# Performance work log

Hardware: AMD Instinct MI355X
Metric: run time of the kernel (lower is better)

Reference implementation:

```python
import jax, jax.numpy as jnp
import numpy as np

N = 16384
E = 524288
F_IN, F_HID, F_OUT = 128, 256, 128
EPS = 1e-5


def setup_inputs() -> dict:
    key = jax.random.key(0)
    ks = jax.random.split(key, 8)
    x = jax.random.normal(ks[0], (N, F_IN), dtype=jnp.float32)
    edge_index = jax.random.randint(ks[1], (2, E), 0, N, dtype=jnp.int64)
    edge_weight = jax.random.uniform(ks[2], (E,), dtype=jnp.float32)
    # Linear params stored as [in, out] (y = x @ W + b; same math as torch Linear)
    W1_w = jax.random.normal(ks[3], (F_IN, F_HID), dtype=jnp.float32) / np.sqrt(F_IN)
    W1_b = jnp.zeros((F_HID,), dtype=jnp.float32)
    W2_w = jax.random.normal(ks[4], (F_HID, F_OUT), dtype=jnp.float32) / np.sqrt(F_HID)
    W2_b = jnp.zeros((F_OUT,), dtype=jnp.float32)
    ln_g = jnp.ones((F_HID,), dtype=jnp.float32)
    ln_b = jnp.zeros((F_HID,), dtype=jnp.float32)
    return {"x": x, "edge_index": edge_index, "edge_weight": edge_weight,
            "W1_w": W1_w, "W1_b": W1_b, "W2_w": W2_w, "W2_b": W2_b,
            "ln_g": ln_g, "ln_b": ln_b}


def _layernorm(h, g, b):
    mu = jnp.mean(h, axis=-1, keepdims=True)
    var = jnp.var(h, axis=-1, keepdims=True)
    return (h - mu) * jax.lax.rsqrt(var + EPS) * g + b


def reference(x, edge_index, edge_weight, W1_w, W1_b, W2_w, W2_b, ln_g, ln_b):
    n = x.shape[0]
    adj = jnp.zeros((n, n), dtype=x.dtype).at[edge_index[0], edge_index[1]].set(edge_weight)
    adj = adj + jnp.eye(n, dtype=x.dtype)
    degree = jnp.clip(adj.sum(axis=1, keepdims=True), 1.0, None)
    adj = adj / degree
    h = jnp.matmul(adj, x) @ W1_w + W1_b          # [N, F_HID]
    h = jax.nn.relu(_layernorm(h, ln_g, ln_b))
    # dropout is identity in eval mode
    out = jnp.matmul(adj, h) @ W2_w + W2_b        # [N, F_OUT]
    return out
```

## Files before the change

kernel.cpp:

```cpp
#include <hip/hip_runtime.h>

#define N_NODES 16384
#define F_IN    128
#define F_HID   256
#define F_OUT   128
#define LN_EPS  1e-5f
#define CAP     96
#define H0STR   136
#define H1STR   264
#define REPSTR  132

typedef __attribute__((ext_vector_type(8))) short bf16x8;
typedef __attribute__((ext_vector_type(4))) float f32x4;
typedef __attribute__((ext_vector_type(4))) int   i32x4;
typedef __attribute__((ext_vector_type(4))) unsigned u32x4;

__device__ __forceinline__ unsigned short bf16rne(float f) {
    unsigned u = __float_as_uint(f);
    unsigned r = (u + 0x7fffu + ((u >> 16) & 1u)) >> 16;
    return (unsigned short)r;
}
__device__ __forceinline__ float bf_lo(unsigned v) { return __uint_as_float(v << 16); }
__device__ __forceinline__ float bf_hi(unsigned v) { return __uint_as_float(v & 0xffff0000u); }

__global__ void pre_small_kernel(int* __restrict__ cur, const unsigned* __restrict__ ei,
                                 int* __restrict__ mode) {
    int b = blockIdx.x, t = threadIdx.x;
    if (b < 64) {
        cur[b * 256 + t] = 0;
    } else {
        __shared__ int nz;
        if (t == 0) nz = 0;
        __syncthreads();
        for (int it = 0; it < 4; ++it) {
            int idx = 2 * (t + it * 256) + 1;
            if (ei[idx] != 0u) nz = 1;
        }
        __syncthreads();
        if (t == 0) *mode = (nz == 0) ? 1 : 0;
    }
}

__global__ void prep_fill_kernel(const void* __restrict__ ei, const int* __restrict__ mode,
                                 int* __restrict__ cur, int2* __restrict__ ed, int E, int nF,
                                 const float* __restrict__ x, unsigned short* __restrict__ xb,
                                 const float* __restrict__ W1, unsigned short* __restrict__ W1t,
                                 const float* __restrict__ W2, unsigned short* __restrict__ W2t) {
    int b = blockIdx.x, t = threadIdx.x;
    if (b < nF) {
        int base = b * 1024 + t;
        int m = *mode;
#pragma unroll
        for (int u = 0; u < 4; ++u) {
            int e = base + u * 256;
            if (e >= E) continue;
            int r, c;
            if (m) {
                const long long* p = (const long long*)ei;
                r = (int)p[e]; c = (int)p[e + E];
            } else {
                const int* p = (const int*)ei;
                r = p[e]; c = p[e + E];
            }
            if (((unsigned)r | (unsigned)c) >= N_NODES) continue;
            int pos = atomicAdd(&cur[r], 1);
            if (pos < CAP) ed[r * CAP + pos] = make_int2(c, e);
        }
    } else if (b < nF + 2048) {
        int i = ((b - nF) * 256 + t) * 4;
        float4 v = *(const float4*)&x[i];
        ushort4 o;
        o.x = bf16rne(v.x); o.y = bf16rne(v.y); o.z = bf16rne(v.z); o.w = bf16rne(v.w);
        *(ushort4*)&xb[i] = o;
    } else if (b < nF + 2176) {
        int id = (b - nF - 2048) * 256 + t;
        int n = id >> 7, k = id & 127;
        W1t[id] = bf16rne(W1[(size_t)k * F_HID + n]);
    } else {
        int id = (b - nF - 2176) * 256 + t;
        int n = id >> 8, k = id & 255;
        W2t[id] = bf16rne(W2[(size_t)k * F_OUT + n]);
    }
}

__launch_bounds__(1024, 8)
__global__ void agg_mlp_kernel(const float* __restrict__ ew, int* __restrict__ cur,
                               int2* __restrict__ ed, float* __restrict__ invdeg,
                               const unsigned* __restrict__ xb,
                               const unsigned short* __restrict__ W1t,
                               const unsigned short* __restrict__ W2t,
                               const float* __restrict__ b1,
                               const float* __restrict__ ln_g, const float* __restrict__ ln_b,
                               unsigned short* __restrict__ h2b) {
    __shared__ int   scol[16][CAP];
    __shared__ int   seid[16][CAP];
    __shared__ float sw[16][CAP];
    __shared__ unsigned short H0[16 * H0STR];
    __shared__ unsigned short H1[16 * H1STR];
    __shared__ float red[2][16][16];

    int t = threadIdx.x, wave = t >> 6, lane = t & 63;
    int lnid = lane & 15, quad = lane >> 4;
    int qw = lane >> 4, ql = lane & 15;
    int Rbase = blockIdx.x * 16;
    int r = Rbase + wave;

    int d = cur[r];
    if (d > CAP) d = CAP;
    int dpad = (d + 15) & ~15;
    int2* row = ed + (size_t)r * CAP;
    for (int i = lane; i < d; i += 64) {
        int2 e = row[i];
        scol[wave][i] = e.x;
        seid[wave][i] = e.y;
    }
    for (int i = d + lane; i < dpad; i += 64) {
        scol[wave][i] = -2;
        seid[wave][i] = 0;
    }
    asm volatile("s_waitcnt lgkmcnt(0)" ::: "memory");

    float wsum = 0.0f;
    for (int i = lane; i < d; i += 64) {
        int myc = scol[wave][i], mye = seid[wave][i];
        bool kill = false;
        for (int jb = 0; jb < dpad; jb += 16) {
            const int* cb = &scol[wave][jb];
            const int* eb = &seid[wave][jb];
            i32x4 c0 = *(const i32x4*)(cb);
            i32x4 c1 = *(const i32x4*)(cb + 4);
            i32x4 c2 = *(const i32x4*)(cb + 8);
            i32x4 c3 = *(const i32x4*)(cb + 12);
            i32x4 e0 = *(const i32x4*)(eb);
            i32x4 e1 = *(const i32x4*)(eb + 4);
            i32x4 e2 = *(const i32x4*)(eb + 8);
            i32x4 e3 = *(const i32x4*)(eb + 12);
            kill |= (c0.x == myc && e0.x > mye);
            kill |= (c0.y == myc && e0.y > mye);
            kill |= (c0.z == myc && e0.z > mye);
            kill |= (c0.w == myc && e0.w > mye);
            kill |= (c1.x == myc && e1.x > mye);
            kill |= (c1.y == myc && e1.y > mye);
            kill |= (c1.z == myc && e1.z > mye);
            kill |= (c1.w == myc && e1.w > mye);
            kill |= (c2.x == myc && e2.x > mye);
            kill |= (c2.y == myc && e2.y > mye);
            kill |= (c2.z == myc && e2.z > mye);
            kill |= (c2.w == myc && e2.w > mye);
            kill |= (c3.x == myc && e3.x > mye);
            kill |= (c3.y == myc && e3.y > mye);
            kill |= (c3.z == myc && e3.z > mye);
            kill |= (c3.w == myc && e3.w > mye);
        }
        float w = kill ? 0.0f : ew[mye];
        sw[wave][i] = w;
        row[i] = make_int2(myc, __float_as_int(w));
        wsum += w;
    }
    asm volatile("s_waitcnt lgkmcnt(0)" ::: "memory");
    for (int off = 32; off; off >>= 1) wsum += __shfl_xor(wsum, off, 64);
    float inv = 1.0f / (1.0f + wsum);
    if (lane == 0) { invdeg[r] = inv; cur[r] = d; }

    const u32x4* xb4 = (const u32x4*)xb;
    float a[8] = {0, 0, 0, 0, 0, 0, 0, 0};
    int j = 0;
    for (; j + 16 <= d; j += 16) {
        int c[4]; float w[4]; u32x4 v[4];
#pragma unroll
        for (int u = 0; u < 4; ++u) {
            int n = j + u * 4 + qw;
            c[u] = scol[wave][n];
            w[u] = sw[wave][n];
        }
#pragma unroll
        for (int u = 0; u < 4; ++u) v[u] = xb4[(size_t)c[u] * 16 + ql];
#pragma unroll
        for (int u = 0; u < 4; ++u)
#pragma unroll
            for (int m = 0; m < 4; ++m) {
                a[2 * m]     += w[u] * bf_lo(v[u][m]);
                a[2 * m + 1] += w[u] * bf_hi(v[u][m]);
            }
    }
    for (; j + 4 <= d; j += 4) {
        int n = j + qw;
        int c = scol[wave][n];
        float w = sw[wave][n];
        u32x4 v = xb4[(size_t)c * 16 + ql];
#pragma unroll
        for (int m = 0; m < 4; ++m) {
            a[2 * m]     += w * bf_lo(v[m]);
            a[2 * m + 1] += w * bf_hi(v[m]);
        }
    }
    int rem = d - j;
    if (rem > 0) {
        int n = j + (qw < rem ? qw : 0);
        float w = (qw < rem) ? sw[wave][n] : 0.0f;
        int c = scol[wave][n];
        u32x4 v = xb4[(size_t)c * 16 + ql];
#pragma unroll
        for (int m = 0; m < 4; ++m) {
            a[2 * m]     += w * bf_lo(v[m]);
            a[2 * m + 1] += w * bf_hi(v[m]);
        }
    }
#pragma unroll
    for (int k = 0; k < 8; ++k) {
        a[k] += __shfl_xor(a[k], 16, 64);
        a[k] += __shfl_xor(a[k], 32, 64);
    }
    if (qw == 0) {
        u32x4 sv = xb4[(size_t)r * 16 + ql];
        u32x4 o;
#pragma unroll
        for (int m = 0; m < 4; ++m) {
            float lo = (a[2 * m]     + bf_lo(sv[m])) * inv;
            float hi = (a[2 * m + 1] + bf_hi(sv[m])) * inv;
            o[m] = ((unsigned)bf16rne(hi) << 16) | (unsigned)bf16rne(lo);
        }
        *(u32x4*)&H0[wave * H0STR + ql * 8] = o;
    }
    __syncthreads();

    bf16x8 afr[4];
#pragma unroll
    for (int ch = 0; ch < 4; ++ch)
        afr[ch] = *(const bf16x8*)&H0[lnid * H0STR + ch * 32 + quad * 8];
    f32x4 acc = {0.0f, 0.0f, 0.0f, 0.0f};
    {
        const unsigned short* wrow = &W1t[(size_t)(wave * 16 + lnid) * F_IN];
#pragma unroll
        for (int ch = 0; ch < 4; ++ch) {
            bf16x8 b = *(const bf16x8*)&wrow[ch * 32 + quad * 8];
            acc = __builtin_amdgcn_mfma_f32_16x16x32_bf16(afr[ch], b, acc, 0, 0, 0);
        }
    }
    float s[4], q[4];
    {
        float bv = b1[wave * 16 + lnid];
#pragma unroll
        for (int rr = 0; rr < 4; ++rr) {
            float v = acc[rr] + bv;
            acc[rr] = v;
            s[rr] = v; q[rr] = v * v;
        }
    }
#pragma unroll
    for (int rr = 0; rr < 4; ++rr)
        for (int off = 1; off < 16; off <<= 1) {
            s[rr] += __shfl_xor(s[rr], off, 64);
            q[rr] += __shfl_xor(q[rr], off, 64);
        }
    if (lnid == 0) {
#pragma unroll
        for (int rr = 0; rr < 4; ++rr) {
            red[0][wave][quad * 4 + rr] = s[rr];
            red[1][wave][quad * 4 + rr] = q[rr];
        }
    }
    __syncthreads();
    float mean[4], rinv[4];
#pragma unroll
    for (int rr = 0; rr < 4; ++rr) {
        int rowi = quad * 4 + rr;
        float S = 0.0f, Q = 0.0f;
#pragma unroll
        for (int w2 = 0; w2 < 16; ++w2) { S += red[0][w2][rowi]; Q += red[1][w2][rowi]; }
        mean[rr] = S * (1.0f / F_HID);
        float var = Q * (1.0f / F_HID) - mean[rr] * mean[rr];
        rinv[rr] = rsqrtf(var + LN_EPS);
    }
    {
        int c = wave * 16 + lnid;
        float g = ln_g[c], bb = ln_b[c];
#pragma unroll
        for (int rr = 0; rr < 4; ++rr) {
            float v = fmaxf((acc[rr] - mean[rr]) * rinv[rr] * g + bb, 0.0f);
            H1[(quad * 4 + rr) * H1STR + c] = bf16rne(v);
        }
    }
    __syncthreads();

    unsigned short* rep = H0;
    if (wave < 8) {
        bf16x8 a2[8];
#pragma unroll
        for (int ch = 0; ch < 8; ++ch)
            a2[ch] = *(const bf16x8*)&H1[lnid * H1STR + ch * 32 + quad * 8];
        f32x4 c2 = {0.0f, 0.0f, 0.0f, 0.0f};
        const unsigned short* wrow = &W2t[(size_t)(wave * 16 + lnid) * F_HID];
#pragma unroll
        for (int ch = 0; ch < 8; ++ch) {
            bf16x8 b = *(const bf16x8*)&wrow[ch * 32 + quad * 8];
            c2 = __builtin_amdgcn_mfma_f32_16x16x32_bf16(a2[ch], b, c2, 0, 0, 0);
        }
#pragma unroll
        for (int rr = 0; rr < 4; ++rr)
            rep[(quad * 4 + rr) * REPSTR + wave * 16 + lnid] = bf16rne(c2[rr]);
    }
    __syncthreads();

    if (t < 512) {
        int m = t >> 5, cg = t & 31;
        *(ushort4*)&h2b[(size_t)(Rbase + m) * F_OUT + cg * 4] =
            *(const ushort4*)&rep[m * REPSTR + cg * 4];
    }
}

__launch_bounds__(1024, 8)
__global__ void spmm2_kernel(const unsigned* __restrict__ xb, const int* __restrict__ cur,
                             const int2* __restrict__ ed, const float* __restrict__ invdeg,
                             const float* __restrict__ bias, float* __restrict__ outp) {
    __shared__ int   scol[16][CAP];
    __shared__ float sw[16][CAP];
    int t = threadIdx.x, wave = t >> 6, lane = t & 63;
    int qw = lane >> 4, ql = lane & 15;
    int r = blockIdx.x * 16 + wave;
    const int2* row = ed + (size_t)r * CAP;
    int d = cur[r];
    if (d > CAP) d = CAP;
    for (int i = lane; i < d; i += 64) {
        int2 e = row[i];
        scol[wave][i] = e.x;
        sw[wave][i] = __int_as_float(e.y);
    }
    asm volatile("s_waitcnt lgkmcnt(0)" ::: "memory");

    const u32x4* xb4 = (const u32x4*)xb;
    float a[8] = {0, 0, 0, 0, 0, 0, 0, 0};
    int j = 0;
    for (; j + 16 <= d; j += 16) {
        int c[4]; float w[4]; u32x4 v[4];
#pragma unroll
        for (int u = 0; u < 4; ++u) {
            int n = j + u * 4 + qw;
            c[u] = scol[wave][n];
            w[u] = sw[wave][n];
        }
#pragma unroll
        for (int u = 0; u < 4; ++u) v[u] = xb4[(size_t)c[u] * 16 + ql];
#pragma unroll
        for (int u = 0; u < 4; ++u)
#pragma unroll
            for (int m = 0; m < 4; ++m) {
                a[2 * m]     += w[u] * bf_lo(v[u][m]);
                a[2 * m + 1] += w[u] * bf_hi(v[u][m]);
            }
    }
    for (; j + 4 <= d; j += 4) {
        int n = j + qw;
        int c = scol[wave][n];
        float w = sw[wave][n];
        u32x4 v = xb4[(size_t)c * 16 + ql];
#pragma unroll
        for (int m = 0; m < 4; ++m) {
            a[2 * m]     += w * bf_lo(v[m]);
            a[2 * m + 1] += w * bf_hi(v[m]);
        }
    }
    int rem = d - j;
    if (rem > 0) {
        int n = j + (qw < rem ? qw : 0);
        float w = (qw < rem) ? sw[wave][n] : 0.0f;
        int c = scol[wave][n];
        u32x4 v = xb4[(size_t)c * 16 + ql];
#pragma unroll
        for (int m = 0; m < 4; ++m) {
            a[2 * m]     += w * bf_lo(v[m]);
            a[2 * m + 1] += w * bf_hi(v[m]);
        }
    }
#pragma unroll
    for (int k = 0; k < 8; ++k) {
        a[k] += __shfl_xor(a[k], 16, 64);
        a[k] += __shfl_xor(a[k], 32, 64);
    }
    if (qw == 0) {
        float inv = invdeg[r];
        u32x4 sv = xb4[(size_t)r * 16 + ql];
        int f = ql * 8;
        f32x4 o0, o1;
#pragma unroll
        for (int m = 0; m < 2; ++m) {
            o0[2 * m]     = (a[2 * m]     + bf_lo(sv[m])) * inv + bias[f + 2 * m];
            o0[2 * m + 1] = (a[2 * m + 1] + bf_hi(sv[m])) * inv + bias[f + 2 * m + 1];
        }
#pragma unroll
        for (int m = 2; m < 4; ++m) {
            o1[2 * m - 4] = (a[2 * m]     + bf_lo(sv[m])) * inv + bias[f + 2 * m];
            o1[2 * m - 3] = (a[2 * m + 1] + bf_hi(sv[m])) * inv + bias[f + 2 * m + 1];
        }
        *(f32x4*)&outp[(size_t)r * F_OUT + f]     = o0;
        *(f32x4*)&outp[(size_t)r * F_OUT + f + 4] = o1;
    }
}

extern "C" void kernel_launch(void* const* d_in, const int* in_sizes, int n_in,
                              void* d_out, int out_size, void* d_ws, size_t ws_size,
                              hipStream_t stream) {
    const float* x   = (const float*)d_in[0];
    const void*  ei  = d_in[1];
    const float* ew  = (const float*)d_in[2];
    const float* W1  = (const float*)d_in[3];
    const float* b1  = (const float*)d_in[4];
    const float* W2  = (const float*)d_in[5];
    const float* b2  = (const float*)d_in[6];
    const float* lng = (const float*)d_in[7];
    const float* lnb = (const float*)d_in[8];
    float* out = (float*)d_out;
    int E = in_sizes[2];

    char* w = (char*)d_ws;
    size_t off = 0;
    auto take = [&](size_t bytes) -> char* {
        char* p = w + off;
        off += (bytes + 255) & ~(size_t)255;
        return p;
    };
    int*   cur    = (int*)take((size_t)N_NODES * 4);
    float* invdeg = (float*)take((size_t)N_NODES * 4);
    int2*  ed     = (int2*)take((size_t)N_NODES * CAP * 8);
    unsigned short* xb  = (unsigned short*)take((size_t)N_NODES * F_IN * 2);
    unsigned short* h2b = (unsigned short*)take((size_t)N_NODES * F_OUT * 2);
    unsigned short* W1t = (unsigned short*)take((size_t)F_IN * F_HID * 2);
    unsigned short* W2t = (unsigned short*)take((size_t)F_HID * F_OUT * 2);
    int*   mode   = (int*)take(4);

    int nF = (E + 1023) / 1024;
    pre_small_kernel<<<65, 256, 0, stream>>>(cur, (const unsigned*)ei, mode);
    prep_fill_kernel<<<nF + 2304, 256, 0, stream>>>(ei, mode, cur, ed, E, nF,
                                                    x, xb, W1, W1t, W2, W2t);
    agg_mlp_kernel<<<N_NODES / 16, 1024, 0, stream>>>(ew, cur, ed, invdeg,
                                                      (const unsigned*)xb, W1t, W2t,
                                                      b1, lng, lnb, h2b);
    spmm2_kernel<<<N_NODES / 16, 1024, 0, stream>>>((const unsigned*)h2b, cur, ed, invdeg,
                                                    b2, out);
}
```

Baseline: 185.3 us.

## Split feature dimension into two planes for cache-friendly sparse aggregation passes

Stores the bf16 node features and the second-layer hidden features as two 64-column planes, and runs each neighbor-gather aggregation as a separate kernel per plane. Each plane is 2 MB instead of 4 MB, so the random gather working set is more likely to stay in L2/LLC. The MLP is split out of the first aggregation kernel into its own kernel that reads both gathered planes. This adds three kernel launches, re-reads the edge lists once per plane, and writes extra intermediate buffers to global memory.

```diff
diff --git a/kernel.cpp b/kernel.cpp
--- a/kernel.cpp
+++ b/kernel.cpp
@@ -9,6 +9,7 @@
 #define H0STR   136
 #define H1STR   264
 #define REPSTR  132
+#define PLANEU  (N_NODES * 32)
 
 typedef __attribute__((ext_vector_type(8))) short bf16x8;
 typedef __attribute__((ext_vector_type(4))) float f32x4;
@@ -71,7 +72,9 @@
         float4 v = *(const float4*)&x[i];
         ushort4 o;
         o.x = bf16rne(v.x); o.y = bf16rne(v.y); o.z = bf16rne(v.z); o.w = bf16rne(v.w);
-        *(ushort4*)&xb[i] = o;
+        int n = i >> 7, f = i & 127;
+        int p = f >> 6, fo = f & 63;
+        *(ushort4*)&xb[(size_t)p * (N_NODES * 64) + n * 64 + fo] = o;
     } else if (b < nF + 2176) {
         int id = (b - nF - 2048) * 256 + t;
         int n = id >> 7, k = id & 127;
@@ -84,26 +87,16 @@
 }
 
 __launch_bounds__(1024, 8)
-__global__ void agg_mlp_kernel(const float* __restrict__ ew, int* __restrict__ cur,
-                               int2* __restrict__ ed, float* __restrict__ invdeg,
-                               const unsigned* __restrict__ xb,
-                               const unsigned short* __restrict__ W1t,
-                               const unsigned short* __restrict__ W2t,
-                               const float* __restrict__ b1,
-                               const float* __restrict__ ln_g, const float* __restrict__ ln_b,
-                               unsigned short* __restrict__ h2b) {
+__global__ void agg_p0_kernel(const float* __restrict__ ew, int* __restrict__ cur,
+                              int2* __restrict__ ed, float* __restrict__ invdeg,
+                              const unsigned* __restrict__ xb,
+                              unsigned short* __restrict__ g0) {
     __shared__ int   scol[16][CAP];
     __shared__ int   seid[16][CAP];
     __shared__ float sw[16][CAP];
-    __shared__ unsigned short H0[16 * H0STR];
-    __shared__ unsigned short H1[16 * H1STR];
-    __shared__ float red[2][16][16];
-
     int t = threadIdx.x, wave = t >> 6, lane = t & 63;
-    int lnid = lane & 15, quad = lane >> 4;
-    int qw = lane >> 4, ql = lane & 15;
-    int Rbase = blockIdx.x * 16;
-    int r = Rbase + wave;
+    int qo = lane >> 3, ql8 = lane & 7;
+    int r = blockIdx.x * 16 + wave;
 
     int d = cur[r];
     if (d > CAP) d = CAP;
@@ -162,19 +155,19 @@
     float inv = 1.0f / (1.0f + wsum);
     if (lane == 0) { invdeg[r] = inv; cur[r] = d; }
 
-    const u32x4* xb4 = (const u32x4*)xb;
+    const u32x4* xp4 = (const u32x4*)xb;
     float a[8] = {0, 0, 0, 0, 0, 0, 0, 0};
     int j = 0;
-    for (; j + 16 <= d; j += 16) {
+    for (; j + 32 <= d; j += 32) {
         int c[4]; float w[4]; u32x4 v[4];
 #pragma unroll
         for (int u = 0; u < 4; ++u) {
-            int n = j + u * 4 + qw;
+            int n = j + u * 8 + qo;
             c[u] = scol[wave][n];
             w[u] = sw[wave][n];
         }
 #pragma unroll
-        for (int u = 0; u < 4; ++u) v[u] = xb4[(size_t)c[u] * 16 + ql];
+        for (int u = 0; u < 4; ++u) v[u] = xp4[(size_t)c[u] * 8 + ql8];
 #pragma unroll
         for (int u = 0; u < 4; ++u)
 #pragma unroll
@@ -183,36 +176,26 @@
                 a[2 * m + 1] += w[u] * bf_hi(v[u][m]);
             }
     }
-    for (; j + 4 <= d; j += 4) {
-        int n = j + qw;
+    for (; j < d; j += 8) {
+        int rem = d - j;
+        int n = j + (qo < rem ? qo : 0);
+        float w = (qo < rem) ? sw[wave][n] : 0.0f;
         int c = scol[wave][n];
-        float w = sw[wave][n];
-        u32x4 v = xb4[(size_t)c * 16 + ql];
+        u32x4 v = xp4[(size_t)c * 8 + ql8];
 #pragma unroll
         for (int m = 0; m < 4; ++m) {
             a[2 * m]     += w * bf_lo(v[m]);
             a[2 * m + 1] += w * bf_hi(v[m]);
         }
     }
-    int rem = d - j;
-    if (rem > 0) {
-        int n = j + (qw < rem ? qw : 0);
-        float w = (qw < rem) ? sw[wave][n] : 0.0f;
-        int c = scol[wave][n];
-        u32x4 v = xb4[(size_t)c * 16 + ql];
-#pragma unroll
-        for (int m = 0; m < 4; ++m) {
-            a[2 * m]     += w * bf_lo(v[m]);
-            a[2 * m + 1] += w * bf_hi(v[m]);
-        }
-    }
 #pragma unroll
     for (int k = 0; k < 8; ++k) {
+        a[k] += __shfl_xor(a[k], 8, 64);
         a[k] += __shfl_xor(a[k], 16, 64);
         a[k] += __shfl_xor(a[k], 32, 64);
     }
-    if (qw == 0) {
-        u32x4 sv = xb4[(size_t)r * 16 + ql];
+    if (qo == 0) {
+        u32x4 sv = xp4[(size_t)r * 8 + ql8];
         u32x4 o;
 #pragma unroll
         for (int m = 0; m < 4; ++m) {
@@ -220,103 +203,19 @@
             float hi = (a[2 * m + 1] + bf_hi(sv[m])) * inv;
             o[m] = ((unsigned)bf16rne(hi) << 16) | (unsigned)bf16rne(lo);
         }
-        *(u32x4*)&H0[wave * H0STR + ql * 8] = o;
-    }
-    __syncthreads();
-
-    bf16x8 afr[4];
-#pragma unroll
-    for (int ch = 0; ch < 4; ++ch)
-        afr[ch] = *(const bf16x8*)&H0[lnid * H0STR + ch * 32 + quad * 8];
-    f32x4 acc = {0.0f, 0.0f, 0.0f, 0.0f};
-    {
-        const unsigned short* wrow = &W1t[(size_t)(wave * 16 + lnid) * F_IN];
-#pragma unroll
-        for (int ch = 0; ch < 4; ++ch) {
-            bf16x8 b = *(const bf16x8*)&wrow[ch * 32 + quad * 8];
-            acc = __builtin_amdgcn_mfma_f32_16x16x32_bf16(afr[ch], b, acc, 0, 0, 0);
-        }
-    }
-    float s[4], q[4];
-    {
-        float bv = b1[wave * 16 + lnid];
-#pragma unroll
-        for (int rr = 0; rr < 4; ++rr) {
-            float v = acc[rr] + bv;
-            acc[rr] = v;
-            s[rr] = v; q[rr] = v * v;
-        }
-    }
-#pragma unroll
-    for (int rr = 0; rr < 4; ++rr)
-        for (int off = 1; off < 16; off <<= 1) {
-            s[rr] += __shfl_xor(s[rr], off, 64);
-            q[rr] += __shfl_xor(q[rr], off, 64);
-        }
-    if (lnid == 0) {
-#pragma unroll
-        for (int rr = 0; rr < 4; ++rr) {
-            red[0][wave][quad * 4 + rr] = s[rr];
-            red[1][wave][quad * 4 + rr] = q[rr];
-        }
-    }
-    __syncthreads();
-    float mean[4], rinv[4];
-#pragma unroll
-    for (int rr = 0; rr < 4; ++rr) {
-        int rowi = quad * 4 + rr;
-        float S = 0.0f, Q = 0.0f;
-#pragma unroll
-        for (int w2 = 0; w2 < 16; ++w2) { S += red[0][w2][rowi]; Q += red[1][w2][rowi]; }
-        mean[rr] = S * (1.0f / F_HID);
-        float var = Q * (1.0f / F_HID) - mean[rr] * mean[rr];
-        rinv[rr] = rsqrtf(var + LN_EPS);
-    }
-    {
-        int c = wave * 16 + lnid;
-        float g = ln_g[c], bb = ln_b[c];
-#pragma unroll
-        for (int rr = 0; rr < 4; ++rr) {
-            float v = fmaxf((acc[rr] - mean[rr]) * rinv[rr] * g + bb, 0.0f);
-            H1[(quad * 4 + rr) * H1STR + c] = bf16rne(v);
-        }
-    }
-    __syncthreads();
-
-    unsigned short* rep = H0;
-    if (wave < 8) {
-        bf16x8 a2[8];
-#pragma unroll
-        for (int ch = 0; ch < 8; ++ch)
-            a2[ch] = *(const bf16x8*)&H1[lnid * H1STR + ch * 32 + quad * 8];
-        f32x4 c2 = {0.0f, 0.0f, 0.0f, 0.0f};
-        const unsigned short* wrow = &W2t[(size_t)(wave * 16 + lnid) * F_HID];
-#pragma unroll
-        for (int ch = 0; ch < 8; ++ch) {
-            bf16x8 b = *(const bf16x8*)&wrow[ch * 32 + quad * 8];
-            c2 = __builtin_amdgcn_mfma_f32_16x16x32_bf16(a2[ch], b, c2, 0, 0, 0);
-        }
-#pragma unroll
-        for (int rr = 0; rr < 4; ++rr)
-            rep[(quad * 4 + rr) * REPSTR + wave * 16 + lnid] = bf16rne(c2[rr]);
-    }
-    __syncthreads();
-
-    if (t < 512) {
-        int m = t >> 5, cg = t & 31;
-        *(ushort4*)&h2b[(size_t)(Rbase + m) * F_OUT + cg * 4] =
-            *(const ushort4*)&rep[m * REPSTR + cg * 4];
+        *(u32x4*)&g0[(size_t)r * 64 + ql8 * 8] = o;
     }
 }
 
 __launch_bounds__(1024, 8)
-__global__ void spmm2_kernel(const unsigned* __restrict__ xb, const int* __restrict__ cur,
-                             const int2* __restrict__ ed, const float* __restrict__ invdeg,
-                             const float* __restrict__ bias, float* __restrict__ outp) {
+__global__ void agg_p1_kernel(const int* __restrict__ cur, const int2* __restrict__ ed,
+                              const float* __restrict__ invdeg,
+                              const unsigned* __restrict__ xb,
+                              unsigned short* __restrict__ g1) {
     __shared__ int   scol[16][CAP];
     __shared__ float sw[16][CAP];
     int t = threadIdx.x, wave = t >> 6, lane = t & 63;
-    int qw = lane >> 4, ql = lane & 15;
+    int qo = lane >> 3, ql8 = lane & 7;
     int r = blockIdx.x * 16 + wave;
     const int2* row = ed + (size_t)r * CAP;
     int d = cur[r];
@@ -327,20 +226,21 @@
         sw[wave][i] = __int_as_float(e.y);
     }
     asm volatile("s_waitcnt lgkmcnt(0)" ::: "memory");
-
-    const u32x4* xb4 = (const u32x4*)xb;
+    float inv = invdeg[r];
+
+    const u32x4* xp4 = (const u32x4*)(xb + PLANEU);
     float a[8] = {0, 0, 0, 0, 0, 0, 0, 0};
     int j = 0;
-    for (; j + 16 <= d; j += 16) {
+    for (; j + 32 <= d; j += 32) {
         int c[4]; float w[4]; u32x4 v[4];
 #pragma unroll
         for (int u = 0; u < 4; ++u) {
-            int n = j + u * 4 + qw;
+            int n = j + u * 8 + qo;
             c[u] = scol[wave][n];
             w[u] = sw[wave][n];
         }
 #pragma unroll
-        for (int u = 0; u < 4; ++u) v[u] = xb4[(size_t)c[u] * 16 + ql];
+        for (int u = 0; u < 4; ++u) v[u] = xp4[(size_t)c[u] * 8 + ql8];
 #pragma unroll
         for (int u = 0; u < 4; ++u)
 #pragma unroll
@@ -349,23 +249,193 @@
                 a[2 * m + 1] += w[u] * bf_hi(v[u][m]);
             }
     }
-    for (; j + 4 <= d; j += 4) {
-        int n = j + qw;
+    for (; j < d; j += 8) {
+        int rem = d - j;
+        int n = j + (qo < rem ? qo : 0);
+        float w = (qo < rem) ? sw[wave][n] : 0.0f;
         int c = scol[wave][n];
-        float w = sw[wave][n];
-        u32x4 v = xb4[(size_t)c * 16 + ql];
+        u32x4 v = xp4[(size_t)c * 8 + ql8];
 #pragma unroll
         for (int m = 0; m < 4; ++m) {
             a[2 * m]     += w * bf_lo(v[m]);
             a[2 * m + 1] += w * bf_hi(v[m]);
         }
     }
-    int rem = d - j;
-    if (rem > 0) {
-        int n = j + (qw < rem ? qw : 0);
-        float w = (qw < rem) ? sw[wave][n] : 0.0f;
+#pragma unroll
+    for (int k = 0; k < 8; ++k) {
+        a[k] += __shfl_xor(a[k], 8, 64);
+        a[k] += __shfl_xor(a[k], 16, 64);
+        a[k] += __shfl_xor(a[k], 32, 64);
+    }
+    if (qo == 0) {
+        u32x4 sv = xp4[(size_t)r * 8 + ql8];
+        u32x4 o;
+#pragma unroll
+        for (int m = 0; m < 4; ++m) {
+            float lo = (a[2 * m]     + bf_lo(sv[m])) * inv;
+            float hi = (a[2 * m + 1] + bf_hi(sv[m])) * inv;
+            o[m] = ((unsigned)bf16rne(hi) << 16) | (unsigned)bf16rne(lo);
+        }
+        *(u32x4*)&g1[(size_t)r * 64 + ql8 * 8] = o;
+    }
+}
+
+__launch_bounds__(1024, 8)
+__global__ void mlp_kernel(const unsigned short* __restrict__ g0,
+                           const unsigned short* __restrict__ g1,
+                           const unsigned short* __restrict__ W1t,
+                           const unsigned short* __restrict__ W2t,
+                           const float* __restrict__ b1,
+                           const float* __restrict__ ln_g, const float* __restrict__ ln_b,
+                           unsigned short* __restrict__ h2b) {
+    __shared__ unsigned short H0[16 * H0STR];
+    __shared__ unsigned short H1[16 * H1STR];
+    __shared__ float red[2][16][16];
+    int t = threadIdx.x, wave = t >> 6, lane = t & 63;
+    int lnid = lane & 15, quad = lane >> 4;
+    int Rbase = blockIdx.x * 16;
+
+    if (t < 512) {
+        int m = t >> 5, cg = t & 31;
+        int p = cg >> 4, fo = (cg & 15) * 4;
+        const unsigned short* src = (p ? g1 : g0) + (size_t)(Rbase + m) * 64 + fo;
+        *(ushort4*)&H0[m * H0STR + p * 64 + fo] = *(const ushort4*)src;
+    }
+    __syncthreads();
+
+    bf16x8 afr[4];
+#pragma unroll
+    for (int ch = 0; ch < 4; ++ch)
+        afr[ch] = *(const bf16x8*)&H0[lnid * H0STR + ch * 32 + quad * 8];
+    f32x4 acc = {0.0f, 0.0f, 0.0f, 0.0f};
+    {
+        const unsigned short* wrow = &W1t[(size_t)(wave * 16 + lnid) * F_IN];
+#pragma unroll
+        for (int ch = 0; ch < 4; ++ch) {
+            bf16x8 b = *(const bf16x8*)&wrow[ch * 32 + quad * 8];
+            acc = __builtin_amdgcn_mfma_f32_16x16x32_bf16(afr[ch], b, acc, 0, 0, 0);
+        }
+    }
+    float s[4], q[4];
+    {
+        float bv = b1[wave * 16 + lnid];
+#pragma unroll
+        for (int rr = 0; rr < 4; ++rr) {
+            float v = acc[rr] + bv;
+            acc[rr] = v;
+            s[rr] = v; q[rr] = v * v;
+        }
+    }
+#pragma unroll
+    for (int rr = 0; rr < 4; ++rr)
+        for (int off = 1; off < 16; off <<= 1) {
+            s[rr] += __shfl_xor(s[rr], off, 64);
+            q[rr] += __shfl_xor(q[rr], off, 64);
+        }
+    if (lnid == 0) {
+#pragma unroll
+        for (int rr = 0; rr < 4; ++rr) {
+            red[0][wave][quad * 4 + rr] = s[rr];
+            red[1][wave][quad * 4 + rr] = q[rr];
+        }
+    }
+    __syncthreads();
+    float mean[4], rinv[4];
+#pragma unroll
+    for (int rr = 0; rr < 4; ++rr) {
+        int rowi = quad * 4 + rr;
+        float S = 0.0f, Q = 0.0f;
+#pragma unroll
+        for (int w2 = 0; w2 < 16; ++w2) { S += red[0][w2][rowi]; Q += red[1][w2][rowi]; }
+        mean[rr] = S * (1.0f / F_HID);
+        float var = Q * (1.0f / F_HID) - mean[rr] * mean[rr];
+        rinv[rr] = rsqrtf(var + LN_EPS);
+    }
+    {
+        int c = wave * 16 + lnid;
+        float g = ln_g[c], bb = ln_b[c];
+#pragma unroll
+        for (int rr = 0; rr < 4; ++rr) {
+            float v = fmaxf((acc[rr] - mean[rr]) * rinv[rr] * g + bb, 0.0f);
+            H1[(quad * 4 + rr) * H1STR + c] = bf16rne(v);
+        }
+    }
+    __syncthreads();
+
+    unsigned short* rep = H0;
+    if (wave < 8) {
+        bf16x8 a2[8];
+#pragma unroll
+        for (int ch = 0; ch < 8; ++ch)
+            a2[ch] = *(const bf16x8*)&H1[lnid * H1STR + ch * 32 + quad * 8];
+        f32x4 c2 = {0.0f, 0.0f, 0.0f, 0.0f};
+        const unsigned short* wrow = &W2t[(size_t)(wave * 16 + lnid) * F_HID];
+#pragma unroll
+        for (int ch = 0; ch < 8; ++ch) {
+            bf16x8 b = *(const bf16x8*)&wrow[ch * 32 + quad * 8];
+            c2 = __builtin_amdgcn_mfma_f32_16x16x32_bf16(a2[ch], b, c2, 0, 0, 0);
+        }
+#pragma unroll
+        for (int rr = 0; rr < 4; ++rr)
+            rep[(quad * 4 + rr) * REPSTR + wave * 16 + lnid] = bf16rne(c2[rr]);
+    }
+    __syncthreads();
+
+    if (t < 512) {
+        int m = t >> 5, cg = t & 31;
+        int p = cg >> 4, fo = (cg & 15) * 4;
+        *(ushort4*)&h2b[(size_t)p * (N_NODES * 64) + (size_t)(Rbase + m) * 64 + fo] =
+            *(const ushort4*)&rep[m * REPSTR + cg * 4];
+    }
+}
+
+__launch_bounds__(1024, 8)
+__global__ void spmm2_p_kernel(const unsigned* __restrict__ h2u, const int* __restrict__ cur,
+                               const int2* __restrict__ ed, const float* __restrict__ invdeg,
+                               const float* __restrict__ bias, float* __restrict__ outp,
+                               int plane) {
+    __shared__ int   scol[16][CAP];
+    __shared__ float sw[16][CAP];
+    int t = threadIdx.x, wave = t >> 6, lane = t & 63;
+    int qo = lane >> 3, ql8 = lane & 7;
+    int r = blockIdx.x * 16 + wave;
+    const int2* row = ed + (size_t)r * CAP;
+    int d = cur[r];
+    if (d > CAP) d = CAP;
+    for (int i = lane; i < d; i += 64) {
+        int2 e = row[i];
+        scol[wave][i] = e.x;
+        sw[wave][i] = __int_as_float(e.y);
+    }
+    asm volatile("s_waitcnt lgkmcnt(0)" ::: "memory");
+
+    const u32x4* xp4 = (const u32x4*)(h2u + (size_t)plane * PLANEU);
+    float a[8] = {0, 0, 0, 0, 0, 0, 0, 0};
+    int j = 0;
+    for (; j + 32 <= d; j += 32) {
+        int c[4]; float w[4]; u32x4 v[4];
+#pragma unroll
+        for (int u = 0; u < 4; ++u) {
+            int n = j + u * 8 + qo;
+            c[u] = scol[wave][n];
+            w[u] = sw[wave][n];
+        }
+#pragma unroll
+        for (int u = 0; u < 4; ++u) v[u] = xp4[(size_t)c[u] * 8 + ql8];
+#pragma unroll
+        for (int u = 0; u < 4; ++u)
+#pragma unroll
+            for (int m = 0; m < 4; ++m) {
+                a[2 * m]     += w[u] * bf_lo(v[u][m]);
+                a[2 * m + 1] += w[u] * bf_hi(v[u][m]);
+            }
+    }
+    for (; j < d; j += 8) {
+        int rem = d - j;
+        int n = j + (qo < rem ? qo : 0);
+        float w = (qo < rem) ? sw[wave][n] : 0.0f;
         int c = scol[wave][n];
-        u32x4 v = xb4[(size_t)c * 16 + ql];
+        u32x4 v = xp4[(size_t)c * 8 + ql8];
 #pragma unroll
         for (int m = 0; m < 4; ++m) {
             a[2 * m]     += w * bf_lo(v[m]);
@@ -374,13 +444,14 @@
     }
 #pragma unroll
     for (int k = 0; k < 8; ++k) {
+        a[k] += __shfl_xor(a[k], 8, 64);
         a[k] += __shfl_xor(a[k], 16, 64);
         a[k] += __shfl_xor(a[k], 32, 64);
     }
-    if (qw == 0) {
+    if (qo == 0) {
         float inv = invdeg[r];
-        u32x4 sv = xb4[(size_t)r * 16 + ql];
-        int f = ql * 8;
+        u32x4 sv = xp4[(size_t)r * 8 + ql8];
+        int f = plane * 64 + ql8 * 8;
         f32x4 o0, o1;
 #pragma unroll
         for (int m = 0; m < 2; ++m) {
@@ -424,6 +495,8 @@
     int2*  ed     = (int2*)take((size_t)N_NODES * CAP * 8);
     unsigned short* xb  = (unsigned short*)take((size_t)N_NODES * F_IN * 2);
     unsigned short* h2b = (unsigned short*)take((size_t)N_NODES * F_OUT * 2);
+    unsigned short* g0  = (unsigned short*)take((size_t)N_NODES * 64 * 2);
+    unsigned short* g1  = (unsigned short*)take((size_t)N_NODES * 64 * 2);
     unsigned short* W1t = (unsigned short*)take((size_t)F_IN * F_HID * 2);
     unsigned short* W2t = (unsigned short*)take((size_t)F_HID * F_OUT * 2);
     int*   mode   = (int*)take(4);
@@ -432,9 +505,13 @@
     pre_small_kernel<<<65, 256, 0, stream>>>(cur, (const unsigned*)ei, mode);
     prep_fill_kernel<<<nF + 2304, 256, 0, stream>>>(ei, mode, cur, ed, E, nF,
                                                     x, xb, W1, W1t, W2, W2t);
-    agg_mlp_kernel<<<N_NODES / 16, 1024, 0, stream>>>(ew, cur, ed, invdeg,
-                                                      (const unsigned*)xb, W1t, W2t,
-                                                      b1, lng, lnb, h2b);
-    spmm2_kernel<<<N_NODES / 16, 1024, 0, stream>>>((const unsigned*)h2b, cur, ed, invdeg,
-                                                    b2, out);
-}
+    agg_p0_kernel<<<N_NODES / 16, 1024, 0, stream>>>(ew, cur, ed, invdeg,
+                                                     (const unsigned*)xb, g0);
+    agg_p1_kernel<<<N_NODES / 16, 1024, 0, stream>>>(cur, ed, invdeg,
+                                                     (const unsigned*)xb, g1);
+    mlp_kernel<<<N_NODES / 16, 1024, 0, stream>>>(g0, g1, W1t, W2t, b1, lng, lnb, h2b);
+    spmm2_p_kernel<<<N_NODES / 16, 1024, 0, stream>>>((const unsigned*)h2b, cur, ed,
+                                                      invdeg, b2, out, 0);
+    spmm2_p_kernel<<<N_NODES / 16, 1024, 0, stream>>>((const unsigned*)h2b, cur, ed,
+                                                      invdeg, b2, out, 1);
+}
```

Result: slower. 200.8 us (+8.4%).

## Fuse all GCN stages into one cooperative persistent kernel with grid syncs

Applied to the files above, without the earlier changes.

Replaces the four-launch pipeline with a single cooperative kernel of 1024 blocks of 512 threads. Grid-wide syncs separate the stages: bf16 conversion and weight transpose, edge bucketing, aggregation plus MLP, and the second SpMM. Each block handles 16 rows with two row passes per wave and keeps per-row degree and inverse degree in registers. This removes launch gaps and the global invdeg and weight write-back between the aggregation and SpMM stages. In exchange it pays for three grid barriers, lowers parallelism per stage, and relies on all 1024 blocks being co-resident, falling back to the old path otherwise.

```diff
diff --git a/kernel.cpp b/kernel.cpp
--- a/kernel.cpp
+++ b/kernel.cpp
@@ -1,4 +1,7 @@
 #include <hip/hip_runtime.h>
+#include <hip/hip_cooperative_groups.h>
+
+namespace cg = cooperative_groups;
 
 #define N_NODES 16384
 #define F_IN    128
@@ -9,6 +12,8 @@
 #define H0STR   136
 #define H1STR   264
 #define REPSTR  132
+#define NB      1024
+#define NT      512
 
 typedef __attribute__((ext_vector_type(8))) short bf16x8;
 typedef __attribute__((ext_vector_type(4))) float f32x4;
@@ -22,6 +27,334 @@
 }
 __device__ __forceinline__ float bf_lo(unsigned v) { return __uint_as_float(v << 16); }
 __device__ __forceinline__ float bf_hi(unsigned v) { return __uint_as_float(v & 0xffff0000u); }
+
+#define QGATHER(lr_, src4_, dd_)                                            \
+    {                                                                       \
+        int j_ = 0;                                                         \
+        for (; j_ + 16 <= (dd_); j_ += 16) {                                \
+            int c_[4]; float w_[4]; u32x4 v_[4];                            \
+            _Pragma("unroll")                                               \
+            for (int u_ = 0; u_ < 4; ++u_) {                                \
+                int n_ = j_ + u_ * 4 + qw;                                  \
+                c_[u_] = scol[lr_][n_];                                     \
+                w_[u_] = sw[lr_][n_];                                       \
+            }                                                               \
+            _Pragma("unroll")                                               \
+            for (int u_ = 0; u_ < 4; ++u_)                                  \
+                v_[u_] = (src4_)[(size_t)c_[u_] * 16 + ql];                 \
+            _Pragma("unroll")                                               \
+            for (int u_ = 0; u_ < 4; ++u_)                                  \
+                _Pragma("unroll")                                           \
+                for (int m_ = 0; m_ < 4; ++m_) {                            \
+                    a[2 * m_]     += w_[u_] * bf_lo(v_[u_][m_]);            \
+                    a[2 * m_ + 1] += w_[u_] * bf_hi(v_[u_][m_]);            \
+                }                                                           \
+        }                                                                   \
+        for (; j_ + 4 <= (dd_); j_ += 4) {                                  \
+            int n_ = j_ + qw;                                               \
+            int c_ = scol[lr_][n_]; float w_ = sw[lr_][n_];                 \
+            u32x4 v_ = (src4_)[(size_t)c_ * 16 + ql];                       \
+            _Pragma("unroll")                                               \
+            for (int m_ = 0; m_ < 4; ++m_) {                                \
+                a[2 * m_]     += w_ * bf_lo(v_[m_]);                        \
+                a[2 * m_ + 1] += w_ * bf_hi(v_[m_]);                        \
+            }                                                               \
+        }                                                                   \
+        int rem_ = (dd_) - j_;                                              \
+        if (rem_ > 0) {                                                     \
+            int n_ = j_ + (qw < rem_ ? qw : 0);                             \
+            float w_ = (qw < rem_) ? sw[lr_][n_] : 0.0f;                    \
+            int c_ = scol[lr_][n_];                                         \
+            u32x4 v_ = (src4_)[(size_t)c_ * 16 + ql];                       \
+            _Pragma("unroll")                                               \
+            for (int m_ = 0; m_ < 4; ++m_) {                                \
+                a[2 * m_]     += w_ * bf_lo(v_[m_]);                        \
+                a[2 * m_ + 1] += w_ * bf_hi(v_[m_]);                        \
+            }                                                               \
+        }                                                                   \
+        _Pragma("unroll")                                                   \
+        for (int k_ = 0; k_ < 8; ++k_) {                                    \
+            a[k_] += __shfl_xor(a[k_], 16, 64);                             \
+            a[k_] += __shfl_xor(a[k_], 32, 64);                             \
+        }                                                                   \
+    }
+
+#define KILL16(lr_, jb_)                                                    \
+    {                                                                       \
+        const int* cb = &scol[lr_][jb_];                                    \
+        const int* eb = &seid[lr_][jb_];                                    \
+        i32x4 c0 = *(const i32x4*)(cb);                                     \
+        i32x4 c1 = *(const i32x4*)(cb + 4);                                 \
+        i32x4 c2 = *(const i32x4*)(cb + 8);                                 \
+        i32x4 c3 = *(const i32x4*)(cb + 12);                                \
+        i32x4 e0 = *(const i32x4*)(eb);                                     \
+        i32x4 e1 = *(const i32x4*)(eb + 4);                                 \
+        i32x4 e2 = *(const i32x4*)(eb + 8);                                 \
+        i32x4 e3 = *(const i32x4*)(eb + 12);                                \
+        kill |= (c0.x == myc && e0.x > mye);                                \
+        kill |= (c0.y == myc && e0.y > mye);                                \
+        kill |= (c0.z == myc && e0.z > mye);                                \
+        kill |= (c0.w == myc && e0.w > mye);                                \
+        kill |= (c1.x == myc && e1.x > mye);                                \
+        kill |= (c1.y == myc && e1.y > mye);                                \
+        kill |= (c1.z == myc && e1.z > mye);                                \
+        kill |= (c1.w == myc && e1.w > mye);                                \
+        kill |= (c2.x == myc && e2.x > mye);                                \
+        kill |= (c2.y == myc && e2.y > mye);                                \
+        kill |= (c2.z == myc && e2.z > mye);                                \
+        kill |= (c2.w == myc && e2.w > mye);                                \
+        kill |= (c3.x == myc && e3.x > mye);                                \
+        kill |= (c3.y == myc && e3.y > mye);                                \
+        kill |= (c3.z == myc && e3.z > mye);                                \
+        kill |= (c3.w == myc && e3.w > mye);                                \
+    }
+
+__launch_bounds__(NT, 8)
+__global__ void gcn_mega(const void* __restrict__ ei, const float* __restrict__ ew,
+                         const float* __restrict__ x,
+                         const float* __restrict__ W1, const float* __restrict__ b1,
+                         const float* __restrict__ W2, const float* __restrict__ b2,
+                         const float* __restrict__ lng, const float* __restrict__ lnb,
+                         int* __restrict__ cur, int2* __restrict__ ed,
+                         unsigned short* __restrict__ xb, unsigned short* __restrict__ h2b,
+                         unsigned short* __restrict__ W1t, unsigned short* __restrict__ W2t,
+                         int* __restrict__ mode, float* __restrict__ out, int E) {
+    __shared__ int   scol[16][CAP];
+    __shared__ int   seid[16][CAP];
+    __shared__ float sw[16][CAP];
+    __shared__ unsigned short H0[16 * H0STR];
+    __shared__ unsigned short H1[16 * H1STR];
+    __shared__ float red[2][8][16];
+    __shared__ int   nzs;
+
+    cg::grid_group grid = cg::this_grid();
+    int t = threadIdx.x, b = blockIdx.x;
+    int gtid = b * NT + t;
+    int wave = t >> 6, lane = t & 63;
+    int lnid = lane & 15, quad = lane >> 4;
+    int qw = lane >> 4, ql = lane & 15;
+
+    {
+        int i = gtid * 4;
+        float4 v = *(const float4*)&x[i];
+        ushort4 o;
+        o.x = bf16rne(v.x); o.y = bf16rne(v.y); o.z = bf16rne(v.z); o.w = bf16rne(v.w);
+        *(ushort4*)&xb[i] = o;
+    }
+    if (gtid < 32768) {
+        int n = gtid >> 7, k = gtid & 127;
+        W1t[gtid] = bf16rne(W1[(size_t)k * F_HID + n]);
+    } else if (gtid < 65536) {
+        int id = gtid - 32768;
+        int n = id >> 8, k = id & 255;
+        W2t[id] = bf16rne(W2[(size_t)k * F_OUT + n]);
+    } else if (gtid < 65536 + N_NODES) {
+        cur[gtid - 65536] = 0;
+    }
+    if (b == NB - 1) {
+        if (t == 0) nzs = 0;
+        __syncthreads();
+        const unsigned* eu = (const unsigned*)ei;
+        for (int it = 0; it < 2; ++it) {
+            int e = t + it * NT;
+            if (e < E && eu[2 * e + 1] != 0u) nzs = 1;
+        }
+        __syncthreads();
+        if (t == 0) *mode = (nzs == 0) ? 1 : 0;
+    }
+    grid.sync();
+
+    {
+        int m = *mode;
+        for (int e = gtid; e < E; e += NB * NT) {
+            int r, c;
+            if (m) {
+                const long long* p = (const long long*)ei;
+                r = (int)p[e]; c = (int)p[e + E];
+            } else {
+                const int* p = (const int*)ei;
+                r = p[e]; c = p[e + E];
+            }
+            if (((unsigned)r | (unsigned)c) >= N_NODES) continue;
+            int pos = atomicAdd(&cur[r], 1);
+            if (pos < CAP) ed[r * CAP + pos] = make_int2(c, e);
+        }
+    }
+    grid.sync();
+
+    int Rbase = b * 16;
+    int dreg[2]; float invreg[2];
+#pragma unroll 1
+    for (int p = 0; p < 2; ++p) {
+        int lr = wave + p * 8;
+        int r = Rbase + lr;
+        int d = cur[r];
+        if (d > CAP) d = CAP;
+        int dpad = (d + 15) & ~15;
+        const int2* row = ed + (size_t)r * CAP;
+        for (int i = lane; i < d; i += 64) {
+            int2 e = row[i];
+            scol[lr][i] = e.x;
+            seid[lr][i] = e.y;
+        }
+        for (int i = d + lane; i < dpad; i += 64) {
+            scol[lr][i] = -2;
+            seid[lr][i] = 0;
+        }
+        asm volatile("s_waitcnt lgkmcnt(0)" ::: "memory");
+
+        float wsum = 0.0f;
+        for (int i = lane; i < d; i += 64) {
+            int myc = scol[lr][i], mye = seid[lr][i];
+            bool kill = false;
+            for (int jb = 0; jb < dpad; jb += 16) KILL16(lr, jb);
+            float w = kill ? 0.0f : ew[mye];
+            sw[lr][i] = w;
+            wsum += w;
+        }
+        asm volatile("s_waitcnt lgkmcnt(0)" ::: "memory");
+        for (int off = 32; off; off >>= 1) wsum += __shfl_xor(wsum, off, 64);
+        float inv = 1.0f / (1.0f + wsum);
+        dreg[p] = d;
+        invreg[p] = inv;
+
+        const u32x4* xb4 = (const u32x4*)xb;
+        float a[8] = {0, 0, 0, 0, 0, 0, 0, 0};
+        QGATHER(lr, xb4, d);
+        if (qw == 0) {
+            u32x4 sv = xb4[(size_t)r * 16 + ql];
+            u32x4 o;
+#pragma unroll
+            for (int m = 0; m < 4; ++m) {
+                float lo = (a[2 * m]     + bf_lo(sv[m])) * inv;
+                float hi = (a[2 * m + 1] + bf_hi(sv[m])) * inv;
+                o[m] = ((unsigned)bf16rne(hi) << 16) | (unsigned)bf16rne(lo);
+            }
+            *(u32x4*)&H0[lr * H0STR + ql * 8] = o;
+        }
+    }
+    __syncthreads();
+
+    {
+        bf16x8 afr[4];
+#pragma unroll
+        for (int ch = 0; ch < 4; ++ch)
+            afr[ch] = *(const bf16x8*)&H0[lnid * H0STR + ch * 32 + quad * 8];
+        f32x4 acc[2];
+#pragma unroll
+        for (int p = 0; p < 2; ++p) {
+            int ct = wave + p * 8;
+            f32x4 c = {0.0f, 0.0f, 0.0f, 0.0f};
+            const unsigned short* wrow = &W1t[(size_t)(ct * 16 + lnid) * F_IN];
+#pragma unroll
+            for (int ch = 0; ch < 4; ++ch) {
+                bf16x8 bb = *(const bf16x8*)&wrow[ch * 32 + quad * 8];
+                c = __builtin_amdgcn_mfma_f32_16x16x32_bf16(afr[ch], bb, c, 0, 0, 0);
+            }
+            acc[p] = c;
+        }
+        float s[4] = {0, 0, 0, 0}, q[4] = {0, 0, 0, 0};
+#pragma unroll
+        for (int p = 0; p < 2; ++p) {
+            float bv = b1[(wave + p * 8) * 16 + lnid];
+#pragma unroll
+            for (int rr = 0; rr < 4; ++rr) {
+                float v = acc[p][rr] + bv;
+                acc[p][rr] = v;
+                s[rr] += v; q[rr] += v * v;
+            }
+        }
+#pragma unroll
+        for (int rr = 0; rr < 4; ++rr)
+            for (int off = 1; off < 16; off <<= 1) {
+                s[rr] += __shfl_xor(s[rr], off, 64);
+                q[rr] += __shfl_xor(q[rr], off, 64);
+            }
+        if (lnid == 0) {
+#pragma unroll
+            for (int rr = 0; rr < 4; ++rr) {
+                red[0][wave][quad * 4 + rr] = s[rr];
+                red[1][wave][quad * 4 + rr] = q[rr];
+            }
+        }
+        __syncthreads();
+        float mean[4], rinv[4];
+#pragma unroll
+        for (int rr = 0; rr < 4; ++rr) {
+            int rowi = quad * 4 + rr;
+            float S = 0.0f, Q = 0.0f;
+#pragma unroll
+            for (int w2 = 0; w2 < 8; ++w2) { S += red[0][w2][rowi]; Q += red[1][w2][rowi]; }
+            mean[rr] = S * (1.0f / F_HID);
+            float var = Q * (1.0f / F_HID) - mean[rr] * mean[rr];
+            rinv[rr] = rsqrtf(var + LN_EPS);
+        }
+#pragma unroll
+        for (int p = 0; p < 2; ++p) {
+            int c = (wave + p * 8) * 16 + lnid;
+            float g = lng[c], bb = lnb[c];
+#pragma unroll
+            for (int rr = 0; rr < 4; ++rr) {
+                float v = fmaxf((acc[p][rr] - mean[rr]) * rinv[rr] * g + bb, 0.0f);
+                H1[(quad * 4 + rr) * H1STR + c] = bf16rne(v);
+            }
+        }
+    }
+    __syncthreads();
+
+    unsigned short* rep = H0;
+    {
+        bf16x8 a2[8];
+#pragma unroll
+        for (int ch = 0; ch < 8; ++ch)
+            a2[ch] = *(const bf16x8*)&H1[lnid * H1STR + ch * 32 + quad * 8];
+        f32x4 c2 = {0.0f, 0.0f, 0.0f, 0.0f};
+        const unsigned short* wrow = &W2t[(size_t)(wave * 16 + lnid) * F_HID];
+#pragma unroll
+        for (int ch = 0; ch < 8; ++ch) {
+            bf16x8 bb = *(const bf16x8*)&wrow[ch * 32 + quad * 8];
+            c2 = __builtin_amdgcn_mfma_f32_16x16x32_bf16(a2[ch], bb, c2, 0, 0, 0);
+        }
+#pragma unroll
+        for (int rr = 0; rr < 4; ++rr)
+            rep[(quad * 4 + rr) * REPSTR + wave * 16 + lnid] = bf16rne(c2[rr]);
+    }
+    __syncthreads();
+    {
+        int m = t >> 5, cgi = t & 31;
+        *(ushort4*)&h2b[(size_t)(Rbase + m) * F_OUT + cgi * 4] =
+            *(const ushort4*)&rep[m * REPSTR + cgi * 4];
+    }
+    grid.sync();
+
+    const u32x4* h24 = (const u32x4*)h2b;
+#pragma unroll 1
+    for (int p = 0; p < 2; ++p) {
+        int lr = wave + p * 8;
+        int r = Rbase + lr;
+        int d = dreg[p];
+        float inv = invreg[p];
+        float a[8] = {0, 0, 0, 0, 0, 0, 0, 0};
+        QGATHER(lr, h24, d);
+        if (qw == 0) {
+            u32x4 sv = h24[(size_t)r * 16 + ql];
+            int f = ql * 8;
+            f32x4 o0, o1;
+#pragma unroll
+            for (int m = 0; m < 2; ++m) {
+                o0[2 * m]     = (a[2 * m]     + bf_lo(sv[m])) * inv + b2[f + 2 * m];
+                o0[2 * m + 1] = (a[2 * m + 1] + bf_hi(sv[m])) * inv + b2[f + 2 * m + 1];
+            }
+#pragma unroll
+            for (int m = 2; m < 4; ++m) {
+                o1[2 * m - 4] = (a[2 * m]     + bf_lo(sv[m])) * inv + b2[f + 2 * m];
+                o1[2 * m - 3] = (a[2 * m + 1] + bf_hi(sv[m])) * inv + b2[f + 2 * m + 1];
+            }
+            *(f32x4*)&out[(size_t)r * F_OUT + f]     = o0;
+            *(f32x4*)&out[(size_t)r * F_OUT + f + 4] = o1;
+        }
+    }
+}
 
 __global__ void pre_small_kernel(int* __restrict__ cur, const unsigned* __restrict__ ei,
                                  int* __restrict__ mode) {
@@ -124,34 +457,7 @@
     for (int i = lane; i < d; i += 64) {
         int myc = scol[wave][i], mye = seid[wave][i];
         bool kill = false;
-        for (int jb = 0; jb < dpad; jb += 16) {
-            const int* cb = &scol[wave][jb];
-            const int* eb = &seid[wave][jb];
-            i32x4 c0 = *(const i32x4*)(cb);
-            i32x4 c1 = *(const i32x4*)(cb + 4);
-            i32x4 c2 = *(const i32x4*)(cb + 8);
-            i32x4 c3 = *(const i32x4*)(cb + 12);
-            i32x4 e0 = *(const i32x4*)(eb);
-            i32x4 e1 = *(const i32x4*)(eb + 4);
-            i32x4 e2 = *(const i32x4*)(eb + 8);
-            i32x4 e3 = *(const i32x4*)(eb + 12);
-            kill |= (c0.x == myc && e0.x > mye);
-            kill |= (c0.y == myc && e0.y > mye);
-            kill |= (c0.z == myc && e0.z > mye);
-            kill |= (c0.w == myc && e0.w > mye);
-            kill |= (c1.x == myc && e1.x > mye);
-            kill |= (c1.y == myc && e1.y > mye);
-            kill |= (c1.z == myc && e1.z > mye);
-            kill |= (c1.w == myc && e1.w > mye);
-            kill |= (c2.x == myc && e2.x > mye);
-            kill |= (c2.y == myc && e2.y > mye);
-            kill |= (c2.z == myc && e2.z > mye);
-            kill |= (c2.w == myc && e2.w > mye);
-            kill |= (c3.x == myc && e3.x > mye);
-            kill |= (c3.y == myc && e3.y > mye);
-            kill |= (c3.z == myc && e3.z > mye);
-            kill |= (c3.w == myc && e3.w > mye);
-        }
+        for (int jb = 0; jb < dpad; jb += 16) KILL16(wave, jb);
         float w = kill ? 0.0f : ew[mye];
         sw[wave][i] = w;
         row[i] = make_int2(myc, __float_as_int(w));
@@ -164,53 +470,7 @@
 
     const u32x4* xb4 = (const u32x4*)xb;
     float a[8] = {0, 0, 0, 0, 0, 0, 0, 0};
-    int j = 0;
-    for (; j + 16 <= d; j += 16) {
-        int c[4]; float w[4]; u32x4 v[4];
-#pragma unroll
-        for (int u = 0; u < 4; ++u) {
-            int n = j + u * 4 + qw;
-            c[u] = scol[wave][n];
-            w[u] = sw[wave][n];
-        }
-#pragma unroll
-        for (int u = 0; u < 4; ++u) v[u] = xb4[(size_t)c[u] * 16 + ql];
-#pragma unroll
-        for (int u = 0; u < 4; ++u)
-#pragma unroll
-            for (int m = 0; m < 4; ++m) {
-                a[2 * m]     += w[u] * bf_lo(v[u][m]);
-                a[2 * m + 1] += w[u] * bf_hi(v[u][m]);
-            }
-    }
-    for (; j + 4 <= d; j += 4) {
-        int n = j + qw;
-        int c = scol[wave][n];
-        float w = sw[wave][n];
-        u32x4 v = xb4[(size_t)c * 16 + ql];
-#pragma unroll
-        for (int m = 0; m < 4; ++m) {
-            a[2 * m]     += w * bf_lo(v[m]);
-            a[2 * m + 1] += w * bf_hi(v[m]);
-        }
-    }
-    int rem = d - j;
-    if (rem > 0) {
-        int n = j + (qw < rem ? qw : 0);
-        float w = (qw < rem) ? sw[wave][n] : 0.0f;
-        int c = scol[wave][n];
-        u32x4 v = xb4[(size_t)c * 16 + ql];
-#pragma unroll
-        for (int m = 0; m < 4; ++m) {
-            a[2 * m]     += w * bf_lo(v[m]);
-            a[2 * m + 1] += w * bf_hi(v[m]);
-        }
-    }
-#pragma unroll
-    for (int k = 0; k < 8; ++k) {
-        a[k] += __shfl_xor(a[k], 16, 64);
-        a[k] += __shfl_xor(a[k], 32, 64);
-    }
+    QGATHER(wave, xb4, d);
     if (qw == 0) {
         u32x4 sv = xb4[(size_t)r * 16 + ql];
         u32x4 o;
@@ -233,8 +493,8 @@
         const unsigned short* wrow = &W1t[(size_t)(wave * 16 + lnid) * F_IN];
 #pragma unroll
         for (int ch = 0; ch < 4; ++ch) {
-            bf16x8 b = *(const bf16x8*)&wrow[ch * 32 + quad * 8];
-            acc = __builtin_amdgcn_mfma_f32_16x16x32_bf16(afr[ch], b, acc, 0, 0, 0);
+            bf16x8 bb = *(const bf16x8*)&wrow[ch * 32 + quad * 8];
+            acc = __builtin_amdgcn_mfma_f32_16x16x32_bf16(afr[ch], bb, acc, 0, 0, 0);
         }
     }
     float s[4], q[4];
@@ -293,8 +553,8 @@
         const unsigned short* wrow = &W2t[(size_t)(wave * 16 + lnid) * F_HID];
 #pragma unroll
         for (int ch = 0; ch < 8; ++ch) {
-            bf16x8 b = *(const bf16x8*)&wrow[ch * 32 + quad * 8];
-            c2 = __builtin_amdgcn_mfma_f32_16x16x32_bf16(a2[ch], b, c2, 0, 0, 0);
+            bf16x8 bb = *(const bf16x8*)&wrow[ch * 32 + quad * 8];
+            c2 = __builtin_amdgcn_mfma_f32_16x16x32_bf16(a2[ch], bb, c2, 0, 0, 0);
         }
 #pragma unroll
         for (int rr = 0; rr < 4; ++rr)
@@ -303,9 +563,9 @@
     __syncthreads();
 
     if (t < 512) {
-        int m = t >> 5, cg = t & 31;
-        *(ushort4*)&h2b[(size_t)(Rbase + m) * F_OUT + cg * 4] =
-            *(const ushort4*)&rep[m * REPSTR + cg * 4];
+        int m = t >> 5, cgi = t & 31;
+        *(ushort4*)&h2b[(size_t)(Rbase + m) * F_OUT + cgi * 4] =
+            *(const ushort4*)&rep[m * REPSTR + cgi * 4];
     }
 }
 
@@ -330,53 +590,7 @@
 
     const u32x4* xb4 = (const u32x4*)xb;
     float a[8] = {0, 0, 0, 0, 0, 0, 0, 0};
-    int j = 0;
-    for (; j + 16 <= d; j += 16) {
-        int c[4]; float w[4]; u32x4 v[4];
-#pragma unroll
-        for (int u = 0; u < 4; ++u) {
-            int n = j + u * 4 + qw;
-            c[u] = scol[wave][n];
-            w[u] = sw[wave][n];
-        }
-#pragma unroll
-        for (int u = 0; u < 4; ++u) v[u] = xb4[(size_t)c[u] * 16 + ql];
-#pragma unroll
-        for (int u = 0; u < 4; ++u)
-#pragma unroll
-            for (int m = 0; m < 4; ++m) {
-                a[2 * m]     += w[u] * bf_lo(v[u][m]);
-                a[2 * m + 1] += w[u] * bf_hi(v[u][m]);
-            }
-    }
-    for (; j + 4 <= d; j += 4) {
-        int n = j + qw;
-        int c = scol[wave][n];
-        float w = sw[wave][n];
-        u32x4 v = xb4[(size_t)c * 16 + ql];
-#pragma unroll
-        for (int m = 0; m < 4; ++m) {
-            a[2 * m]     += w * bf_lo(v[m]);
-            a[2 * m + 1] += w * bf_hi(v[m]);
-        }
-    }
-    int rem = d - j;
-    if (rem > 0) {
-        int n = j + (qw < rem ? qw : 0);
-        float w = (qw < rem) ? sw[wave][n] : 0.0f;
-        int c = scol[wave][n];
-        u32x4 v = xb4[(size_t)c * 16 + ql];
-#pragma unroll
-        for (int m = 0; m < 4; ++m) {
-            a[2 * m]     += w * bf_lo(v[m]);
-            a[2 * m + 1] += w * bf_hi(v[m]);
-        }
-    }
-#pragma unroll
-    for (int k = 0; k < 8; ++k) {
-        a[k] += __shfl_xor(a[k], 16, 64);
-        a[k] += __shfl_xor(a[k], 32, 64);
-    }
+    QGATHER(wave, xb4, d);
     if (qw == 0) {
         float inv = invdeg[r];
         u32x4 sv = xb4[(size_t)r * 16 + ql];
@@ -400,8 +614,8 @@
 extern "C" void kernel_launch(void* const* d_in, const int* in_sizes, int n_in,
                               void* d_out, int out_size, void* d_ws, size_t ws_size,
                               hipStream_t stream) {
+    const void*  ei  = d_in[1];
     const float* x   = (const float*)d_in[0];
-    const void*  ei  = d_in[1];
     const float* ew  = (const float*)d_in[2];
     const float* W1  = (const float*)d_in[3];
     const float* b1  = (const float*)d_in[4];
@@ -428,6 +642,26 @@
     unsigned short* W2t = (unsigned short*)take((size_t)F_HID * F_OUT * 2);
     int*   mode   = (int*)take(4);
 
+    static int coop = -1;
+    if (coop < 0) {
+        int nb = 0;
+        if (hipOccupancyMaxActiveBlocksPerMultiprocessor(&nb, gcn_mega, NT, 0)
+                != hipSuccess)
+            nb = 0;
+        coop = (nb >= 4) ? 1 : 0;
+    }
+    if (coop) {
+        void* args[] = {(void*)&ei, (void*)&ew, (void*)&x, (void*)&W1, (void*)&b1,
+                        (void*)&W2, (void*)&b2, (void*)&lng, (void*)&lnb,
+                        (void*)&cur, (void*)&ed, (void*)&xb, (void*)&h2b,
+                        (void*)&W1t, (void*)&W2t, (void*)&mode, (void*)&out, (void*)&E};
+        hipError_t err = hipLaunchCooperativeKernel((void*)gcn_mega, dim3(NB), dim3(NT),
+                                                    args, 0, stream);
+        if (err == hipSuccess) return;
+        (void)hipGetLastError();
+        coop = 0;
+    }
+
     int nF = (E + 1023) / 1024;
     pre_small_kernel<<<65, 256, 0, stream>>>(cur, (const unsigned*)ei, mode);
     prep_fill_kernel<<<nF + 2304, 256, 0, stream>>>(ei, mode, cur, ed, E, nF,
```

New measurement: 186.3 us. No clear change (+0.5%).
